# Performance work log

Measured on AMD Instinct MI355X. Metric: run time of the kernel, lower is better.

Reference implementation:

```python
import jax, jax.numpy as jnp
import numpy as np
from jax import lax

T, D, H, O = 16384, 257, 512, 257


def setup_inputs() -> dict:
    key = jax.random.key(0)
    ks = jax.random.split(key, 7)
    s = 1.0 / np.sqrt(H)  # PyTorch LSTM/Linear uniform init scale
    u = lambda k, shp: jax.random.uniform(k, shp, jnp.float32, -s, s)
    return {
        "stft": jax.random.normal(ks[0], (T, D), jnp.float32),
        "W_ih": u(ks[1], (4 * H, D)),
        "W_hh": u(ks[2], (4 * H, H)),
        "b_ih": u(ks[3], (4 * H,)),
        "b_hh": u(ks[4], (4 * H,)),
        "W_out": u(ks[5], (O, H)),
        "b_out": u(ks[6], (O,)),
    }


def reference(stft, W_ih, W_hh, b_ih, b_hh, W_out, b_out):
    # Batch size is 1 (stft.view(T, 1, -1)), so we scan over [T, D] directly.
    # Precompute input-to-gate GEMM for all timesteps: [T, 4H]
    x_gates = stft @ W_ih.T + (b_ih + b_hh)

    def step(carry, xg):
        h, c = carry  # [H], [H]
        g = xg + h @ W_hh.T  # [4H], PyTorch gate order: i, f, g, o
        i, f, gg, o = jnp.split(g, 4)
        i = jax.nn.sigmoid(i)
        f = jax.nn.sigmoid(f)
        gg = jnp.tanh(gg)
        o = jax.nn.sigmoid(o)
        c = f * c + i * gg
        h = o * jnp.tanh(c)
        return (h, c), h

    h0 = jnp.zeros((H,), stft.dtype)  # init_hidden(): zeros
    c0 = jnp.zeros((H,), stft.dtype)
    _, hs = lax.scan(step, (h0, c0), x_gates)  # hs: [T, H]

    out_space = hs @ W_out.T + b_out  # [T, O]
    return jax.nn.log_softmax(out_space, axis=1)
```

## Files before the change

### kernel.cpp

```cpp
#include <hip/hip_runtime.h>
#include <cmath>

#define T_STEPS 16384
#define D_IN    257
#define H_DIM   512
#define O_DIM   257
#define G4      2048

typedef unsigned long long u64;

#define WS_XG_OFF     8192
#define WS_HS_OFF     (8192 + (size_t)T_STEPS * G4 * 4)

__device__ inline float fast_sigmoid(float x) {
    return 1.f / (1.f + __expf(-x));
}
__device__ inline float fast_tanh(float x) {
    float ax = fminf(fabsf(x), 15.f);
    float e  = __expf(2.f * ax);
    float t  = (e - 1.f) / (e + 1.f);
    return copysignf(t, x);
}
__device__ inline float dot4(float4 a, float4 b) {
    return a.x * b.x + a.y * b.y + a.z * b.z + a.w * b.w;
}

#define PIN4(v) asm volatile("" : "+v"(v.x), "+v"(v.y), "+v"(v.z), "+v"(v.w))

__global__ __launch_bounds__(256) void xgate_gemm(
    const float* __restrict__ stft, const float* __restrict__ W_ih,
    const float* __restrict__ b_ih, const float* __restrict__ b_hh,
    float* __restrict__ xg)
{
    const int tid = threadIdx.x;
    const int tx = tid & 15, ty = tid >> 4;
    const int j0 = blockIdx.x * 64;
    const int t0 = blockIdx.y * 64;

    __shared__ float s_a[64][17];
    __shared__ float s_b[64][17];

    float acc[4][4] = {};

    for (int k0 = 0; k0 < D_IN; k0 += 16) {
        #pragma unroll
        for (int l = 0; l < 4; ++l) {
            int idx = tid + l * 256;
            int r  = idx >> 4;
            int kk = idx & 15;
            int k  = k0 + kk;
            s_a[r][kk] = (k < D_IN) ? stft[(size_t)(t0 + r) * D_IN + k] : 0.f;
            s_b[r][kk] = (k < D_IN) ? W_ih[(size_t)(j0 + r) * D_IN + k] : 0.f;
        }
        __syncthreads();
        #pragma unroll
        for (int kk = 0; kk < 16; ++kk) {
            float a[4], b[4];
            #pragma unroll
            for (int r = 0; r < 4; ++r) a[r] = s_a[ty * 4 + r][kk];
            #pragma unroll
            for (int c = 0; c < 4; ++c) b[c] = s_b[tx * 4 + c][kk];
            #pragma unroll
            for (int r = 0; r < 4; ++r)
                #pragma unroll
                for (int c = 0; c < 4; ++c)
                    acc[r][c] += a[r] * b[c];
        }
        __syncthreads();
    }

    float bias[4];
    #pragma unroll
    for (int c = 0; c < 4; ++c) {
        int j = j0 + tx * 4 + c;
        bias[c] = b_ih[j] + b_hh[j];
    }
    #pragma unroll
    for (int r = 0; r < 4; ++r) {
        int t = t0 + ty * 4 + r;
        #pragma unroll
        for (int c = 0; c < 4; ++c) {
            xg[(size_t)t * G4 + j0 + tx * 4 + c] = acc[r][c] + bias[c];
        }
    }
}

__global__ __launch_bounds__(512, 1) void lstm_seq(
    const float* __restrict__ W_hh, const float* __restrict__ xg,
    float* __restrict__ hs, u64* __restrict__ msg)
{
    const int tid  = threadIdx.x;
    const int g    = blockIdx.x;
    const int w    = tid >> 6;
    const int lane = tid & 63;
    const int j    = lane >> 2;
    const int c    = lane & 3;
    const int colb = w * 64 + c * 16;

    const float* wbase = W_hh + (size_t)(g * 16 + j) * H_DIM + colb;
    const size_t gstride = (size_t)H_DIM * H_DIM;
    float4 wA0, wA1, wA2, wA3, wB0, wB1, wB2, wB3;
    float4 wC0, wC1, wC2, wC3, wD0, wD1, wD2, wD3;
    {
        const float4* p0 = (const float4*)(wbase);
        const float4* p1 = (const float4*)(wbase + gstride);
        const float4* p2 = (const float4*)(wbase + 2 * gstride);
        const float4* p3 = (const float4*)(wbase + 3 * gstride);
        wA0 = p0[0]; wA1 = p0[1]; wA2 = p0[2]; wA3 = p0[3];
        wB0 = p1[0]; wB1 = p1[1]; wB2 = p1[2]; wB3 = p1[3];
        wC0 = p2[0]; wC1 = p2[1]; wC2 = p2[2]; wC3 = p2[3];
        wD0 = p3[0]; wD1 = p3[1]; wD2 = p3[2]; wD3 = p3[3];
    }
    PIN4(wA0); PIN4(wA1); PIN4(wA2); PIN4(wA3);
    PIN4(wB0); PIN4(wB1); PIN4(wB2); PIN4(wB3);
    PIN4(wC0); PIN4(wC1); PIN4(wC2); PIN4(wC3);
    PIN4(wD0); PIN4(wD1); PIN4(wD2); PIN4(wD3);

    __shared__ float s_h[512];
    __shared__ float s_part[2][512];

    u64* slot0 = msg;
    u64* slot1 = msg + 512;

    float c_state = 0.f;
    const int t_j = lane & 15;

    for (int t = 0; t < T_STEPS; ++t) {
        const unsigned tagt = (unsigned)t;
        const int buf = t & 1;

        float xv = 0.f;
        if (w == 0)
            xv = __builtin_nontemporal_load(
                xg + (size_t)t * G4 + (lane >> 4) * H_DIM + g * 16 + t_j);

        u64* rp = (buf ? slot1 : slot0) + tid;
        u64 u;
        for (;;) {
            u = __hip_atomic_load(rp, __ATOMIC_RELAXED, __HIP_MEMORY_SCOPE_AGENT);
            if ((unsigned)(u >> 32) == tagt) break;
        }

        s_h[tid] = __uint_as_float((unsigned)u);

        const float4* hv = (const float4*)(s_h + colb);
        float4 h0 = hv[0], h1 = hv[1], h2 = hv[2], h3 = hv[3];

        float p0 = dot4(wA0, h0) + dot4(wA1, h1) + dot4(wA2, h2) + dot4(wA3, h3);
        float p1 = dot4(wB0, h0) + dot4(wB1, h1) + dot4(wB2, h2) + dot4(wB3, h3);
        float p2 = dot4(wC0, h0) + dot4(wC1, h1) + dot4(wC2, h2) + dot4(wC3, h3);
        float p3 = dot4(wD0, h0) + dot4(wD1, h1) + dot4(wD2, h2) + dot4(wD3, h3);

        const bool lo2 = (c < 2);
        float a0 = (lo2 ? p0 : p2) + __shfl_xor(lo2 ? p2 : p0, 2, 64);
        float a1 = (lo2 ? p1 : p3) + __shfl_xor(lo2 ? p3 : p1, 2, 64);
        const bool ev = ((c & 1) == 0);
        float fin = (ev ? a0 : a1) + __shfl_xor(ev ? a1 : a0, 1, 64);

        s_part[buf][w * 64 + c * 16 + j] = fin;

        asm volatile("s_waitcnt lgkmcnt(0)\n\ts_barrier" ::: "memory");

        if (w == 0) {
            const float* pp = &s_part[buf][0];
            float sum = xv;
            #pragma unroll
            for (int k = 0; k < 8; ++k) sum += pp[k * 64 + lane];

            float gi = __shfl(sum, t_j + 0,  64);
            float gf = __shfl(sum, t_j + 16, 64);
            float gg = __shfl(sum, t_j + 32, 64);
            float go = __shfl(sum, t_j + 48, 64);

            float iv = fast_sigmoid(gi);
            float fv = fast_sigmoid(gf);
            float ov = fast_sigmoid(go);
            float gv = fast_tanh(gg);
            c_state = fv * c_state + iv * gv;
            float hn = ov * fast_tanh(c_state);

            if (lane < 16) {
                __builtin_nontemporal_store(hn, hs + (size_t)t * H_DIM + g * 16 + lane);
                u64 m = ((u64)(tagt + 1) << 32) | (u64)__float_as_uint(hn);
                u64* wp = (((t + 1) & 1) ? slot1 : slot0) + (g * 16 + lane);
                __hip_atomic_store(wp, m, __ATOMIC_RELAXED, __HIP_MEMORY_SCOPE_AGENT);
            }
        }
    }
}

__global__ __launch_bounds__(256) void out_softmax(
    const float* __restrict__ hs, const float* __restrict__ W_out,
    const float* __restrict__ b_out, float* __restrict__ out)
{
    const int tid = threadIdx.x;
    const int t0  = blockIdx.x * 16;

    __shared__ float s_w[257 * 33];
    __shared__ float s_hs[16 * 33];
    __shared__ float s_o[16 * 257];
    __shared__ float s_red[8];

    float acc[16] = {};
    float acc256 = 0.f;

    for (int k0 = 0; k0 < H_DIM; k0 += 32) {
        for (int idx = tid; idx < 257 * 32; idx += 256) {
            int row = idx >> 5, col = idx & 31;
            s_w[row * 33 + col] = W_out[(size_t)row * H_DIM + k0 + col];
        }
        for (int idx = tid; idx < 16 * 32; idx += 256) {
            int row = idx >> 5, col = idx & 31;
            s_hs[row * 33 + col] = hs[(size_t)(t0 + row) * H_DIM + k0 + col];
        }
        __syncthreads();
        #pragma unroll
        for (int kk = 0; kk < 32; ++kk) {
            float w = s_w[tid * 33 + kk];
            #pragma unroll
            for (int r = 0; r < 16; ++r)
                acc[r] += s_hs[r * 33 + kk] * w;
        }
        if (tid < 16) {
            #pragma unroll
            for (int kk = 0; kk < 32; ++kk)
                acc256 += s_w[256 * 33 + kk] * s_hs[tid * 33 + kk];
        }
        __syncthreads();
    }

    float bias_c = b_out[tid];
    #pragma unroll
    for (int r = 0; r < 16; ++r) s_o[r * 257 + tid] = acc[r] + bias_c;
    if (tid < 16) s_o[tid * 257 + 256] = acc256 + b_out[256];
    __syncthreads();

    const int lane = tid & 63, wid = tid >> 6;
    for (int r = 0; r < 16; ++r) {
        float v  = s_o[r * 257 + tid];
        float vx = (tid == 0) ? s_o[r * 257 + 256] : -INFINITY;
        float m = fmaxf(v, vx);
        #pragma unroll
        for (int off = 32; off > 0; off >>= 1) m = fmaxf(m, __shfl_xor(m, off, 64));
        if (lane == 0) s_red[wid] = m;
        __syncthreads();
        m = fmaxf(fmaxf(s_red[0], s_red[1]), fmaxf(s_red[2], s_red[3]));
        float e = expf(v - m) + ((tid == 0) ? expf(vx - m) : 0.f);
        #pragma unroll
        for (int off = 32; off > 0; off >>= 1) e += __shfl_xor(e, off, 64);
        if (lane == 0) s_red[4 + wid] = e;
        __syncthreads();
        float s = s_red[4] + s_red[5] + s_red[6] + s_red[7];
        float lg = logf(s) + m;
        out[(size_t)(t0 + r) * O_DIM + tid] = v - lg;
        if (tid == 0) out[(size_t)(t0 + r) * O_DIM + 256] = vx - lg;
    }
}

extern "C" void kernel_launch(void* const* d_in, const int* in_sizes, int n_in,
                              void* d_out, int out_size, void* d_ws, size_t ws_size,
                              hipStream_t stream) {
    (void)in_sizes; (void)n_in; (void)out_size; (void)ws_size;

    const float* stft  = (const float*)d_in[0];
    const float* W_ih  = (const float*)d_in[1];
    const float* W_hh  = (const float*)d_in[2];
    const float* b_ih  = (const float*)d_in[3];
    const float* b_hh  = (const float*)d_in[4];
    const float* W_out = (const float*)d_in[5];
    const float* b_out = (const float*)d_in[6];
    float* out = (float*)d_out;

    char* ws = (char*)d_ws;
    u64* msg  = (u64*)ws;
    float* xg = (float*)(ws + WS_XG_OFF);
    float* hs = (float*)(ws + WS_HS_OFF);

    (void)hipMemsetAsync(ws, 0, 8192, stream);

    xgate_gemm<<<dim3(G4 / 64, T_STEPS / 64), 256, 0, stream>>>(
        stft, W_ih, b_ih, b_hh, xg);
    lstm_seq<<<32, 512, 0, stream>>>(W_hh, xg, hs, msg);
    out_softmax<<<T_STEPS / 16, 256, 0, stream>>>(hs, W_out, b_out, out);
}
```

Measured before the change: 24.70 ms.

## Co-locate LSTM recurrence blocks on one XCC to keep handoff in local L2

The recurrent kernel now launches 256 blocks, each padded with large shared memory so only one fits per CU. Each block reads its XCC id, and the first XCC to gather 32 blocks claims the recurrence; all other blocks exit. Per-step h exchange then uses L2-coherent (sc0) loads and stores inside that XCC, with a system-coherent mirror copy and a spin-count fallback in case of a stall. The next step's xg value is also prefetched before the spin-wait. The aim is to cut cross-XCC coherence latency on every step. The cost is extra blocks launched and exiting, plus reliance on co-residency assumptions that may hang or fall back if fewer than 32 blocks land on one XCC.

After: 42.86 ms. 73.6% more time.

```diff
diff --git a/kernel.cpp b/kernel.cpp
--- a/kernel.cpp
+++ b/kernel.cpp
@@ -9,8 +9,9 @@
 
 typedef unsigned long long u64;
 
-#define WS_XG_OFF     8192
-#define WS_HS_OFF     (8192 + (size_t)T_STEPS * G4 * 4)
+#define WS_CTL_OFF    16384
+#define WS_XG_OFF     16640
+#define WS_HS_OFF     (WS_XG_OFF + (size_t)T_STEPS * G4 * 4)
 
 __device__ inline float fast_sigmoid(float x) {
     return 1.f / (1.f + __expf(-x));
@@ -87,10 +88,42 @@
 
 __global__ __launch_bounds__(512, 1) void lstm_seq(
     const float* __restrict__ W_hh, const float* __restrict__ xg,
-    float* __restrict__ hs, u64* __restrict__ msg)
+    float* __restrict__ hs, u64* __restrict__ msg, unsigned* __restrict__ ctl)
 {
+    __shared__ int   s_pad[28672];
+    __shared__ float s_h[512];
+    __shared__ float s_part[2][512];
+
     const int tid  = threadIdx.x;
-    const int g    = blockIdx.x;
+
+    int xcc;
+    asm volatile("s_getreg_b32 %0, hwreg(HW_REG_XCC_ID)" : "=s"(xcc));
+    xcc &= 7;
+
+    if (tid == 0) {
+        int role = -1;
+        unsigned idx = __hip_atomic_fetch_add(&ctl[xcc], 1u,
+                          __ATOMIC_RELAXED, __HIP_MEMORY_SCOPE_AGENT);
+        if (idx < 32) {
+            if (idx == 31) {
+                unsigned exp0 = 0;
+                __hip_atomic_compare_exchange_strong(&ctl[8], &exp0,
+                    (unsigned)(xcc + 1), __ATOMIC_RELAXED, __ATOMIC_RELAXED,
+                    __HIP_MEMORY_SCOPE_AGENT);
+            }
+            unsigned wv;
+            do {
+                wv = __hip_atomic_load(&ctl[8], __ATOMIC_RELAXED,
+                                       __HIP_MEMORY_SCOPE_AGENT);
+            } while (wv == 0);
+            if (wv == (unsigned)(xcc + 1)) role = (int)idx;
+        }
+        s_pad[0] = role;
+    }
+    __syncthreads();
+    const int g = s_pad[0];
+    if (g < 0) return;
+
     const int w    = tid >> 6;
     const int lane = tid & 63;
     const int j    = lane >> 2;
@@ -116,29 +149,54 @@
     PIN4(wC0); PIN4(wC1); PIN4(wC2); PIN4(wC3);
     PIN4(wD0); PIN4(wD1); PIN4(wD2); PIN4(wD3);
 
-    __shared__ float s_h[512];
-    __shared__ float s_part[2][512];
-
-    u64* slot0 = msg;
-    u64* slot1 = msg + 512;
-
     float c_state = 0.f;
     const int t_j = lane & 15;
+
+    const u64 adA0 = (u64)(uintptr_t)(msg + tid);
+    const u64 adA1 = (u64)(uintptr_t)(msg + 512 + tid);
+    bool use_fb = false;
+
+    float xv_next = 0.f;
+    if (w == 0)
+        xv_next = __builtin_nontemporal_load(
+            xg + (size_t)0 * G4 + (lane >> 4) * H_DIM + g * 16 + t_j);
 
     for (int t = 0; t < T_STEPS; ++t) {
         const unsigned tagt = (unsigned)t;
         const int buf = t & 1;
 
-        float xv = 0.f;
-        if (w == 0)
-            xv = __builtin_nontemporal_load(
-                xg + (size_t)t * G4 + (lane >> 4) * H_DIM + g * 16 + t_j);
-
-        u64* rp = (buf ? slot1 : slot0) + tid;
+        const float xv = xv_next;
+
         u64 u;
-        for (;;) {
-            u = __hip_atomic_load(rp, __ATOMIC_RELAXED, __HIP_MEMORY_SCOPE_AGENT);
-            if ((unsigned)(u >> 32) == tagt) break;
+        {
+            const u64 adA = buf ? adA1 : adA0;
+            if (!use_fb) {
+                int spins = 0;
+                for (;;) {
+                    asm volatile(
+                        "global_load_dwordx2 %0, %1, off sc0\n\t"
+                        "s_waitcnt vmcnt(0)"
+                        : "=v"(u) : "v"(adA) : "memory");
+                    if ((unsigned)(u >> 32) == tagt) break;
+                    if (++spins > 32768) { use_fb = true; break; }
+                }
+            }
+            if (use_fb) {
+                const u64 adB = adA + 8192;
+                for (;;) {
+                    asm volatile(
+                        "global_load_dwordx2 %0, %1, off sc0 sc1\n\t"
+                        "s_waitcnt vmcnt(0)"
+                        : "=v"(u) : "v"(adB) : "memory");
+                    if ((unsigned)(u >> 32) == tagt) break;
+                }
+            }
+        }
+
+        if (w == 0) {
+            int tn = (t + 1 < T_STEPS) ? t + 1 : t;
+            xv_next = __builtin_nontemporal_load(
+                xg + (size_t)tn * G4 + (lane >> 4) * H_DIM + g * 16 + t_j);
         }
 
         s_h[tid] = __uint_as_float((unsigned)u);
@@ -180,10 +238,15 @@
             float hn = ov * fast_tanh(c_state);
 
             if (lane < 16) {
+                u64 m = ((u64)(tagt + 1) << 32) | (u64)__float_as_uint(hn);
+                u64* wpA = msg + (((t + 1) & 1) ? 512 : 0) + (g * 16 + lane);
+                u64 aA = (u64)(uintptr_t)wpA;
+                u64 aB = aA + 8192;
+                asm volatile("global_store_dwordx2 %0, %1, off"
+                             :: "v"(aA), "v"(m) : "memory");
+                asm volatile("global_store_dwordx2 %0, %1, off sc0 sc1"
+                             :: "v"(aB), "v"(m) : "memory");
                 __builtin_nontemporal_store(hn, hs + (size_t)t * H_DIM + g * 16 + lane);
-                u64 m = ((u64)(tagt + 1) << 32) | (u64)__float_as_uint(hn);
-                u64* wp = (((t + 1) & 1) ? slot1 : slot0) + (g * 16 + lane);
-                __hip_atomic_store(wp, m, __ATOMIC_RELAXED, __HIP_MEMORY_SCOPE_AGENT);
             }
         }
     }
@@ -272,14 +335,15 @@
     float* out = (float*)d_out;
 
     char* ws = (char*)d_ws;
-    u64* msg  = (u64*)ws;
-    float* xg = (float*)(ws + WS_XG_OFF);
-    float* hs = (float*)(ws + WS_HS_OFF);
-
-    (void)hipMemsetAsync(ws, 0, 8192, stream);
+    u64* msg      = (u64*)ws;
+    unsigned* ctl = (unsigned*)(ws + WS_CTL_OFF);
+    float* xg     = (float*)(ws + WS_XG_OFF);
+    float* hs     = (float*)(ws + WS_HS_OFF);
+
+    (void)hipMemsetAsync(ws, 0, WS_XG_OFF, stream);
 
     xgate_gemm<<<dim3(G4 / 64, T_STEPS / 64), 256, 0, stream>>>(
         stft, W_ih, b_ih, b_hh, xg);
-    lstm_seq<<<32, 512, 0, stream>>>(W_hh, xg, hs, msg);
+    lstm_seq<<<256, 512, 0, stream>>>(W_hh, xg, hs, msg, ctl);
     out_softmax<<<T_STEPS / 16, 256, 0, stream>>>(hs, W_out, b_out, out);
 }
```

## Restructure LSTM step so each wave owns two hidden units and reduces in-wave

Applied to the files above, without the earlier changes.

Each wave now holds the full 512-wide rows of W_hh for two hidden units across all four gates, so the per-step dot product is reduced entirely with cross-lane shuffles inside the wave. This removes the shared-memory partial-sum exchange and the single-wave gate computation that previously serialized the tail of each step behind wave 0. The h vector is double-buffered in shared memory, leaving one barrier per step. The reduction needs more shuffle stages, and every wave now computes activations and publishes its own outputs.

New measurement: 38.19 ms. 1.55x slower.

```diff
diff --git a/kernel.cpp b/kernel.cpp
--- a/kernel.cpp
+++ b/kernel.cpp
@@ -93,46 +93,35 @@
     const int g    = blockIdx.x;
     const int w    = tid >> 6;
     const int lane = tid & 63;
-    const int j    = lane >> 2;
-    const int c    = lane & 3;
-    const int colb = w * 64 + c * 16;
-
-    const float* wbase = W_hh + (size_t)(g * 16 + j) * H_DIM + colb;
-    const size_t gstride = (size_t)H_DIM * H_DIM;
-    float4 wA0, wA1, wA2, wA3, wB0, wB1, wB2, wB3;
-    float4 wC0, wC1, wC2, wC3, wD0, wD1, wD2, wD3;
-    {
-        const float4* p0 = (const float4*)(wbase);
-        const float4* p1 = (const float4*)(wbase + gstride);
-        const float4* p2 = (const float4*)(wbase + 2 * gstride);
-        const float4* p3 = (const float4*)(wbase + 3 * gstride);
-        wA0 = p0[0]; wA1 = p0[1]; wA2 = p0[2]; wA3 = p0[3];
-        wB0 = p1[0]; wB1 = p1[1]; wB2 = p1[2]; wB3 = p1[3];
-        wC0 = p2[0]; wC1 = p2[1]; wC2 = p2[2]; wC3 = p2[3];
-        wD0 = p3[0]; wD1 = p3[1]; wD2 = p3[2]; wD3 = p3[3];
-    }
-    PIN4(wA0); PIN4(wA1); PIN4(wA2); PIN4(wA3);
-    PIN4(wB0); PIN4(wB1); PIN4(wB2); PIN4(wB3);
-    PIN4(wC0); PIN4(wC1); PIN4(wC2); PIN4(wC3);
-    PIN4(wD0); PIN4(wD1); PIN4(wD2); PIN4(wD3);
-
-    __shared__ float s_h[512];
-    __shared__ float s_part[2][512];
+
+    const int gate = ((lane & 1) << 1) | ((lane >> 1) & 1);
+    const int jbit = (lane >> 2) & 1;
+    const int jloc = 2 * w + jbit;
+
+    float4 wv[16];
+    #pragma unroll
+    for (int i = 0; i < 8; ++i) {
+        size_t R = (size_t)(i >> 1) * H_DIM + (size_t)(g * 16 + 2 * w + (i & 1));
+        const float4* p = (const float4*)(W_hh + R * H_DIM + 8 * lane);
+        wv[2 * i]     = p[0];
+        wv[2 * i + 1] = p[1];
+    }
+    #pragma unroll
+    for (int i = 0; i < 16; ++i) PIN4(wv[i]);
+
+    __shared__ float s_h[2][512];
 
     u64* slot0 = msg;
     u64* slot1 = msg + 512;
 
     float c_state = 0.f;
-    const int t_j = lane & 15;
+    const int xoff = gate * H_DIM + g * 16 + jloc;
 
     for (int t = 0; t < T_STEPS; ++t) {
         const unsigned tagt = (unsigned)t;
         const int buf = t & 1;
 
-        float xv = 0.f;
-        if (w == 0)
-            xv = __builtin_nontemporal_load(
-                xg + (size_t)t * G4 + (lane >> 4) * H_DIM + g * 16 + t_j);
+        float xv = __builtin_nontemporal_load(xg + (size_t)t * G4 + xoff);
 
         u64* rp = (buf ? slot1 : slot0) + tid;
         u64 u;
@@ -140,51 +129,60 @@
             u = __hip_atomic_load(rp, __ATOMIC_RELAXED, __HIP_MEMORY_SCOPE_AGENT);
             if ((unsigned)(u >> 32) == tagt) break;
         }
-
-        s_h[tid] = __uint_as_float((unsigned)u);
-
-        const float4* hv = (const float4*)(s_h + colb);
-        float4 h0 = hv[0], h1 = hv[1], h2 = hv[2], h3 = hv[3];
-
-        float p0 = dot4(wA0, h0) + dot4(wA1, h1) + dot4(wA2, h2) + dot4(wA3, h3);
-        float p1 = dot4(wB0, h0) + dot4(wB1, h1) + dot4(wB2, h2) + dot4(wB3, h3);
-        float p2 = dot4(wC0, h0) + dot4(wC1, h1) + dot4(wC2, h2) + dot4(wC3, h3);
-        float p3 = dot4(wD0, h0) + dot4(wD1, h1) + dot4(wD2, h2) + dot4(wD3, h3);
-
-        const bool lo2 = (c < 2);
-        float a0 = (lo2 ? p0 : p2) + __shfl_xor(lo2 ? p2 : p0, 2, 64);
-        float a1 = (lo2 ? p1 : p3) + __shfl_xor(lo2 ? p3 : p1, 2, 64);
-        const bool ev = ((c & 1) == 0);
-        float fin = (ev ? a0 : a1) + __shfl_xor(ev ? a1 : a0, 1, 64);
-
-        s_part[buf][w * 64 + c * 16 + j] = fin;
+        s_h[buf][tid] = __uint_as_float((unsigned)u);
 
         asm volatile("s_waitcnt lgkmcnt(0)\n\ts_barrier" ::: "memory");
 
-        if (w == 0) {
-            const float* pp = &s_part[buf][0];
-            float sum = xv;
-            #pragma unroll
-            for (int k = 0; k < 8; ++k) sum += pp[k * 64 + lane];
-
-            float gi = __shfl(sum, t_j + 0,  64);
-            float gf = __shfl(sum, t_j + 16, 64);
-            float gg = __shfl(sum, t_j + 32, 64);
-            float go = __shfl(sum, t_j + 48, 64);
-
-            float iv = fast_sigmoid(gi);
-            float fv = fast_sigmoid(gf);
-            float ov = fast_sigmoid(go);
-            float gv = fast_tanh(gg);
-            c_state = fv * c_state + iv * gv;
-            float hn = ov * fast_tanh(c_state);
-
-            if (lane < 16) {
-                __builtin_nontemporal_store(hn, hs + (size_t)t * H_DIM + g * 16 + lane);
-                u64 m = ((u64)(tagt + 1) << 32) | (u64)__float_as_uint(hn);
-                u64* wp = (((t + 1) & 1) ? slot1 : slot0) + (g * 16 + lane);
-                __hip_atomic_store(wp, m, __ATOMIC_RELAXED, __HIP_MEMORY_SCOPE_AGENT);
+        const float4* hv = (const float4*)(&s_h[buf][8 * lane]);
+        float4 hA = hv[0], hB = hv[1];
+        float p[8];
+        #pragma unroll
+        for (int i = 0; i < 8; ++i)
+            p[i] = dot4(wv[2 * i], hA) + dot4(wv[2 * i + 1], hB);
+
+        float sum;
+        {
+            const bool b0 = lane & 1;
+            float q[4];
+            #pragma unroll
+            for (int i = 0; i < 4; ++i) {
+                float keep = b0 ? p[i + 4] : p[i];
+                float send = b0 ? p[i]     : p[i + 4];
+                q[i] = keep + __shfl_xor(send, 1, 64);
             }
+            const bool b1 = lane & 2;
+            float r2[2];
+            #pragma unroll
+            for (int i = 0; i < 2; ++i) {
+                float keep = b1 ? q[i + 2] : q[i];
+                float send = b1 ? q[i]     : q[i + 2];
+                r2[i] = keep + __shfl_xor(send, 2, 64);
+            }
+            const bool b2 = lane & 4;
+            float keep = b2 ? r2[1] : r2[0];
+            float send = b2 ? r2[0] : r2[1];
+            float s = keep + __shfl_xor(send, 4, 64);
+            s += __shfl_xor(s, 8, 64);
+            s += __shfl_xor(s, 16, 64);
+            s += __shfl_xor(s, 32, 64);
+            sum = s + xv;
+        }
+
+        float act = (gate == 2) ? fast_tanh(sum) : fast_sigmoid(sum);
+        const int lbase = lane & ~3;
+        float iv = __shfl(act, lbase | 0, 64);
+        float fv = __shfl(act, lbase | 2, 64);
+        float gv = __shfl(act, lbase | 1, 64);
+        float ov = __shfl(act, lbase | 3, 64);
+
+        c_state = fv * c_state + iv * gv;
+        float hn = ov * fast_tanh(c_state);
+
+        if (lane == 0 || lane == 4) {
+            u64 m = ((u64)(tagt + 1) << 32) | (u64)__float_as_uint(hn);
+            u64* wp = (((t + 1) & 1) ? slot1 : slot0) + (g * 16 + jloc);
+            __hip_atomic_store(wp, m, __ATOMIC_RELAXED, __HIP_MEMORY_SCOPE_AGENT);
+            __builtin_nontemporal_store(hn, hs + (size_t)t * H_DIM + g * 16 + jloc);
         }
     }
 }
```
